# Kernel optimization log

Measured on AMD Instinct MI355X. Metric: run time of the kernel, lower is better.

Reference implementation:

```python
import jax, jax.numpy as jnp
import numpy as np

N = 30000      # num_nodes
R0 = 8         # original relations
R = 2 * R0 + 1 # with inverses + self-loop relation = 17
IN = 256
OUT = 256
E = 300000     # original triples
NB = 8         # num_bases


def setup_inputs() -> dict:
    key = jax.random.key(0)
    k1, k2, k3, k4, k5, k6 = jax.random.split(key, 6)
    s = jax.random.randint(k1, (E,), 0, N)
    r = jax.random.randint(k2, (E,), 0, R0)
    o = jax.random.randint(k3, (E,), 0, N)
    triples = jnp.stack([s, r, o], axis=1)  # [E,3] int
    features = jax.random.normal(k4, (N, IN), dtype=jnp.float32)
    bases = jax.random.normal(k5, (NB, IN, OUT), dtype=jnp.float32) * 0.02
    comps = jax.random.normal(k6, (R, NB), dtype=jnp.float32) * 0.02
    bias = jnp.zeros((OUT,), dtype=jnp.float32)
    return {"triples": triples, "features": features, "bases": bases, "comps": comps, "bias": bias}


def reference(triples, features, bases, comps, bias):
    # basis decomposition: weights[r] = sum_b comps[r,b] * bases[b]
    weights = jnp.einsum('rb,bio->rio', comps, bases)  # [R, IN, OUT]

    s, r, o = triples[:, 0], triples[:, 1], triples[:, 2]
    nodes = jnp.arange(N)
    # eval mode: self_loop_keep_prob = 1 -> all N self loops kept
    src = jnp.concatenate([s, o, nodes])                                  # [E + E + N]
    rel = jnp.concatenate([r, r + R0, jnp.full((N,), 2 * R0, r.dtype)])
    dst = jnp.concatenate([o, s, nodes])

    # horizontal stacking: adj is [N, R*N]; row = src, col = rel*N + dst
    cols = rel * N + dst
    # column normalisation (row_normalisation=False branch of sum_sparse)
    col_sums = jnp.zeros((R * N,), jnp.float32).at[cols].add(1.0)
    sums = col_sums[cols]
    # reorder: swap normalizers of original and inverse edge blocks
    sums = jnp.concatenate([sums[E:2 * E], sums[:E], sums[2 * E:]])
    vals = 1.0 / sums

    # fw[r*N + n] = features[n] @ weights[r]
    fw = jnp.einsum('ni,rio->rno', features, weights).reshape(R * N, OUT)
    msgs = vals[:, None] * fw[cols]                    # [num_edges, OUT]
    out = jnp.zeros((N, OUT), jnp.float32).at[src].add(msgs)
    return out + bias
```

## Files before the change

### kernel.cpp

```cpp
#include <hip/hip_runtime.h>


namespace {
constexpr int kN     = 30000;
constexpr int kR0    = 8;
constexpr int kNRel  = 16;
constexpr int kIN    = 256;
constexpr int kOUT   = 256;
constexpr int kE     = 300000;
constexpr int kNB    = 8;
constexpr int kKT    = kNB * kIN;
constexpr int kRows  = kN * kNRel;
constexpr int kMsgs  = 2 * kE;
constexpr int kScanBlk  = 1024;
constexpr int kNScanBlk = (kRows + kScanBlk - 1) / kScanBlk;
constexpr int kBM    = 64;
constexpr int kMB    = (kN + kBM - 1) / kBM;
constexpr int kMPad  = kMB * kBM;
constexpr int kTN    = 16;
}

typedef __bf16 bf16x8 __attribute__((ext_vector_type(8)));
typedef float  f32x4  __attribute__((ext_vector_type(4)));
typedef float  f32x2  __attribute__((ext_vector_type(2)));
typedef float  f32x4v __attribute__((ext_vector_type(4)));
typedef unsigned int u32;

static __device__ __forceinline__ ushort f2bf(float x) {
  unsigned u = __float_as_uint(x);
  u += 0x7FFF + ((u >> 16) & 1);
  return (ushort)(u >> 16);
}

static __device__ __forceinline__ void gload16(const void* g, void* l) {
  __builtin_amdgcn_global_load_lds(
      (const __attribute__((address_space(1))) u32*)g,
      (__attribute__((address_space(3))) u32*)l, 16, 0, 0);
}

#define PKFMA_LO(ACC, G, C) \
  asm("v_pk_fma_f32 %0, %1, %2, %0 op_sel_hi:[1,0,1]" : "+v"(ACC) : "v"(G), "v"(C))
#define PKFMA_HI(ACC, G, C) \
  asm("v_pk_fma_f32 %0, %1, %2, %0 op_sel:[0,1,0] op_sel_hi:[1,1,1]" : "+v"(ACC) : "v"(G), "v"(C))


__global__ void k_prep(const float* __restrict__ f, ushort* __restrict__ fb,
                       const int* __restrict__ t, int* __restrict__ deg) {
  int i = blockIdx.x * 256 + threadIdx.x;
  if (i < kN * kIN / 4) {
    float4 v = reinterpret_cast<const float4*>(f)[i];
    ushort4 p;
    p.x = f2bf(v.x); p.y = f2bf(v.y); p.z = f2bf(v.z); p.w = f2bf(v.w);
    reinterpret_cast<ushort4*>(fb)[i] = p;
  }
  if (i < kE) {
    int s = t[3*i], r = t[3*i+1], o = t[3*i+2];
    atomicAdd(&deg[s * kNRel + r], 1);
    atomicAdd(&deg[o * kNRel + kR0 + r], 1);
  }
}

__global__ void k_bt(const float* __restrict__ bases, ushort* __restrict__ Bt) {
  __shared__ float tile[16][256];
  int b = blockIdx.x;
  int t = threadIdx.x;
#pragma unroll
  for (int kk = 0; kk < 16; ++kk)
    tile[kk][t] = bases[(size_t)(b * 16 + kk) * kOUT + t];
  __syncthreads();
  char* dst = (char*)Bt + (size_t)t * 4096;
  int xr = (t & 7) << 4;
#pragma unroll
  for (int q = 0; q < 4; ++q) {
    ushort4 p;
    p.x = f2bf(tile[q*4+0][t]); p.y = f2bf(tile[q*4+1][t]);
    p.z = f2bf(tile[q*4+2][t]); p.w = f2bf(tile[q*4+3][t]);
    *reinterpret_cast<ushort4*>(dst + ((b * 32 + q * 8) ^ xr)) = p;
  }
}


__global__ void k_scan1(const int* __restrict__ deg, int* __restrict__ rp,
                        int* __restrict__ blksum) {
  __shared__ int s[256];
  int tid = threadIdx.x;
  int base = blockIdx.x * kScanBlk + tid * 4;
  int v0 = 0, v1 = 0, v2 = 0, v3 = 0;
  if (base + 3 < kRows) {
    v0 = deg[base]; v1 = deg[base+1]; v2 = deg[base+2]; v3 = deg[base+3];
  } else {
    if (base     < kRows) v0 = deg[base];
    if (base + 1 < kRows) v1 = deg[base+1];
    if (base + 2 < kRows) v2 = deg[base+2];
  }
  int t0 = v0, t1 = t0 + v1, t2 = t1 + v2, t3 = t2 + v3;
  s[tid] = t3;
  __syncthreads();
  for (int off = 1; off < 256; off <<= 1) {
    int x = 0;
    if (tid >= off) x = s[tid - off];
    __syncthreads();
    s[tid] += x;
    __syncthreads();
  }
  int excl = tid ? s[tid-1] : 0;
  if (base     < kRows) rp[base]   = excl;
  if (base + 1 < kRows) rp[base+1] = excl + t0;
  if (base + 2 < kRows) rp[base+2] = excl + t1;
  if (base + 3 < kRows) rp[base+3] = excl + t2;
  if (tid == 255) blksum[blockIdx.x] = s[255];
}

__global__ void k_scan2(int* __restrict__ blksum) {
  __shared__ int s[512];
  int tid = threadIdx.x;
  s[tid] = (tid < kNScanBlk) ? blksum[tid] : 0;
  __syncthreads();
  for (int off = 1; off < 512; off <<= 1) {
    int x = 0;
    if (tid >= off) x = s[tid - off];
    __syncthreads();
    s[tid] += x;
    __syncthreads();
  }
  if (tid < kNScanBlk) blksum[tid] = tid ? s[tid-1] : 0;
}

__global__ void k_scan3(int* __restrict__ rp, const int* __restrict__ blksum) {
  int i = blockIdx.x * 256 + threadIdx.x;
  if (i < kRows)       rp[i] += blksum[i >> 10];
  else if (i == kRows) rp[i]  = kMsgs;
}

__global__ void k_scatter(const int* __restrict__ t, const int* __restrict__ rp,
                          int* __restrict__ deg, int* __restrict__ col) {
  int m = blockIdx.x * 256 + threadIdx.x;
  if (m >= kMsgs) return;
  int e = (m < kE) ? m : m - kE;
  int s = t[3*e], r = t[3*e+1], o = t[3*e+2];
  int rr, tn, sn;
  if (m < kE) { rr = r;        tn = s; sn = o; }
  else        { rr = kR0 + r;  tn = o; sn = s; }
  int idx = tn * kNRel + rr;
  int pos = rp[idx] + (atomicSub(&deg[idx], 1) - 1);
  col[pos] = (rr << 16) | sn;
}

#define FMA4(A, S, G) \
  A.x += (S) * G.x; A.y += (S) * G.y; A.z += (S) * G.z; A.w += (S) * G.w;


__global__ __launch_bounds__(256, 6)
void k_agg1(const int* __restrict__ rp, const int* __restrict__ col,
            const ushort* __restrict__ featbf, const float* __restrict__ comps,
            ushort* __restrict__ aggb) {
  __shared__ float cvb[4][17][kNB];
  int wv   = threadIdx.x >> 6;
  int lane = threadIdx.x & 63;
  int node = blockIdx.x * 4 + wv;

  if (lane < 17) {
    float val = 0.f;
    if (lane < kNRel) {
      int idx = node * kNRel + lane;
      int d = rp[idx + 1] - rp[idx];
      val = d > 0 ? 1.0f / (float)d : 0.f;
    }
#pragma unroll
    for (int b = 0; b < kNB; ++b)
      cvb[wv][lane][b] = comps[lane * kNB + b] * val;
  }
  __syncthreads();

  int se0 = __builtin_amdgcn_readfirstlane(rp[node * kNRel]);
  int se1 = __builtin_amdgcn_readfirstlane(rp[node * kNRel + kNRel]);

  f32x2 accp[2 * kNB];
  {
    uint2 sf = *reinterpret_cast<const uint2*>(featbf + (size_t)node * kIN + lane * 4);
    f32x2 p01, p23;
    p01.x = __uint_as_float(sf.x << 16);
    p01.y = __uint_as_float(sf.x & 0xFFFF0000u);
    p23.x = __uint_as_float(sf.y << 16);
    p23.y = __uint_as_float(sf.y & 0xFFFF0000u);
#pragma unroll
    for (int b = 0; b < kNB; ++b) {
      float cs = comps[2*kR0*kNB + b];
      accp[2*b]     = p01 * cs;
      accp[2*b + 1] = p23 * cs;
    }
  }

  const int pad = (16 << 16);
  int voff = lane * 4;

  int sc[4];
#pragma unroll
  for (int j = 0; j < 4; ++j) {
    int ee = se0 + j;
    int ic = ee < se1 ? ee : 0;
    int v  = col[ic];
    sc[j] = ee < se1 ? v : pad;
  }

  for (int e = se0; e < se1; e += 4) {
    uint2 g[4];
#pragma unroll
    for (int j = 0; j < 4; ++j) {
      const ushort* rowp = featbf + (size_t)(sc[j] & 0xFFFF) * kIN;
      g[j] = *reinterpret_cast<const uint2*>(rowp + voff);
    }
    int sr[4];
#pragma unroll
    for (int j = 0; j < 4; ++j) sr[j] = sc[j] >> 16;
#pragma unroll
    for (int j = 0; j < 4; ++j) {
      int ee = e + 4 + j;
      int ic = ee < se1 ? ee : 0;
      int v  = col[ic];
      sc[j] = ee < se1 ? v : pad;
    }
#pragma unroll
    for (int j = 0; j < 4; ++j) {
      f32x4v cA = *reinterpret_cast<const f32x4v*>(&cvb[wv][sr[j]][0]);
      f32x4v cB = *reinterpret_cast<const f32x4v*>(&cvb[wv][sr[j]][4]);
      f32x2 p01, p23;
      p01.x = __uint_as_float(g[j].x << 16);
      p01.y = __uint_as_float(g[j].x & 0xFFFF0000u);
      p23.x = __uint_as_float(g[j].y << 16);
      p23.y = __uint_as_float(g[j].y & 0xFFFF0000u);
      f32x2 cAl = cA.lo, cAh = cA.hi, cBl = cB.lo, cBh = cB.hi;
      PKFMA_LO(accp[0],  p01, cAl); PKFMA_LO(accp[1],  p23, cAl);
      PKFMA_HI(accp[2],  p01, cAl); PKFMA_HI(accp[3],  p23, cAl);
      PKFMA_LO(accp[4],  p01, cAh); PKFMA_LO(accp[5],  p23, cAh);
      PKFMA_HI(accp[6],  p01, cAh); PKFMA_HI(accp[7],  p23, cAh);
      PKFMA_LO(accp[8],  p01, cBl); PKFMA_LO(accp[9],  p23, cBl);
      PKFMA_HI(accp[10], p01, cBl); PKFMA_HI(accp[11], p23, cBl);
      PKFMA_LO(accp[12], p01, cBh); PKFMA_LO(accp[13], p23, cBh);
      PKFMA_HI(accp[14], p01, cBh); PKFMA_HI(accp[15], p23, cBh);
    }
  }

  char* rowp = (char*)aggb + (size_t)node * 4096;
  int xr = (node & 7) << 4;
#pragma unroll
  for (int b = 0; b < kNB; ++b) {
    ushort4 p;
    p.x = f2bf(accp[2*b].x);     p.y = f2bf(accp[2*b].y);
    p.z = f2bf(accp[2*b + 1].x); p.w = f2bf(accp[2*b + 1].y);
    *reinterpret_cast<ushort4*>(rowp + ((b * 512 + lane * 8) ^ xr)) = p;
  }
}


__global__ __launch_bounds__(512, 4)
void k_gemm(const ushort* __restrict__ aggb, const ushort* __restrict__ Bt,
            const float* __restrict__ bias, float* __restrict__ out) {
  __shared__ ushort Albs[2][kBM * 64];
  __shared__ ushort Blds[2][256 * 64];
  int tid  = threadIdx.x;
  int wv   = tid >> 6;
  int lane = tid & 63;
  int mh   = wv >> 2;
  int nq   = wv & 3;
  int l15  = lane & 15;
  int g4   = lane >> 4;
  int node0 = blockIdx.x * kBM;

  f32x4 acc[2][4];
#pragma unroll
  for (int mt = 0; mt < 2; ++mt)
#pragma unroll
    for (int nt = 0; nt < 4; ++nt) acc[mt][nt] = f32x4{0.f, 0.f, 0.f, 0.f};

  auto stage = [&](int c, int buf) {
    {
      int lin = wv * 1024 + lane * 16;
      int row = lin >> 7;
      const char* src = (const char*)aggb + (size_t)(node0 + row) * 4096
                        + c * 128 + (lin & 127);
      gload16(src, (char*)Albs[buf] + wv * 1024);
    }
#pragma unroll
    for (int i = 0; i < 4; ++i) {
      int seg = wv * 4 + i;
      int lin = seg * 1024 + lane * 16;
      int colr = lin >> 7;
      const char* src = (const char*)Bt + (size_t)colr * 4096
                        + c * 128 + (lin & 127);
      gload16(src, (char*)Blds[buf] + seg * 1024);
    }
  };

  stage(0, 0);
  asm volatile("s_waitcnt vmcnt(0)" ::: "memory");
  __syncthreads();

  int cur = 0;
  for (int c = 0; c < 32; ++c) {
    if (c + 1 < 32) stage(c + 1, cur ^ 1);
#pragma unroll
    for (int ks = 0; ks < 2; ++ks) {
      int kb = ks * 64 + g4 * 16;
      bf16x8 a[2], b[4];
#pragma unroll
      for (int mt = 0; mt < 2; ++mt) {
        int row = mh * 32 + mt * 16 + l15;
        a[mt] = *reinterpret_cast<const bf16x8*>(
            (const char*)Albs[cur] + row * 128 + (kb ^ ((row & 7) << 4)));
      }
#pragma unroll
      for (int nt = 0; nt < 4; ++nt) {
        int colr = nq * 64 + nt * 16 + l15;
        b[nt] = *reinterpret_cast<const bf16x8*>(
            (const char*)Blds[cur] + colr * 128 + (kb ^ ((colr & 7) << 4)));
      }
#pragma unroll
      for (int mt = 0; mt < 2; ++mt)
#pragma unroll
        for (int nt = 0; nt < 4; ++nt)
          acc[mt][nt] = __builtin_amdgcn_mfma_f32_16x16x32_bf16(a[mt], b[nt],
                                                                acc[mt][nt], 0, 0, 0);
    }
    asm volatile("s_waitcnt vmcnt(0)" ::: "memory");
    __syncthreads();
    cur ^= 1;
  }

#pragma unroll
  for (int nt = 0; nt < 4; ++nt) {
    int colo = nq * 64 + nt * 16 + l15;
    float bi = bias[colo];
#pragma unroll
    for (int mt = 0; mt < 2; ++mt) {
      int rbase = node0 + mh * 32 + mt * 16 + g4 * 4;
#pragma unroll
      for (int j = 0; j < 4; ++j) {
        int row = rbase + j;
        if (row < kN) out[(size_t)row * kOUT + colo] = acc[mt][nt][j] + bi;
      }
    }
  }
}


__global__ __launch_bounds__(512, 4)
void k_out_fused(const int* __restrict__ rp, const int* __restrict__ col,
                 const float* __restrict__ feat, const ushort* __restrict__ featbf,
                 const ushort* __restrict__ Bt, const float* __restrict__ comps,
                 const float* __restrict__ bias, float* __restrict__ out) {
  __shared__ ushort aggs[kTN * kKT];
  __shared__ float  cvb[kTN][17][kNB];
  int tid  = threadIdx.x;
  int wv   = tid >> 6;
  int lane = tid & 63;
  int node0 = blockIdx.x * kTN;

  for (int q = tid; q < kTN * 17; q += 512) {
    int nl = q / 17, rl = q - nl * 17;
    float val = 0.f;
    if (rl < kNRel) {
      int idx = (node0 + nl) * kNRel + rl;
      int d = rp[idx + 1] - rp[idx];
      val = d > 0 ? 1.0f / (float)d : 0.f;
    }
#pragma unroll
    for (int b = 0; b < kNB; ++b)
      cvb[nl][rl][b] = comps[rl * kNB + b] * val;
  }
  __syncthreads();

  for (int half = 0; half < 2; ++half) {
    int nl   = (wv << 1) | half;
    int node = node0 + nl;
    int e0 = rp[node * kNRel];
    int e1 = rp[node * kNRel + kNRel];

    float4 f = *reinterpret_cast<const float4*>(feat + (size_t)node * kIN + lane * 4);
    float4 acc[kNB];
#pragma unroll
    for (int b = 0; b < kNB; ++b) {
      float cs = comps[2*kR0*kNB + b];
      acc[b].x = cs * f.x; acc[b].y = cs * f.y; acc[b].z = cs * f.z; acc[b].w = cs * f.w;
    }
    const float4* cvr = reinterpret_cast<const float4*>(&cvb[nl][0][0]);
    const int pad = (16 << 16);
    int cc[4];
#pragma unroll
    for (int j = 0; j < 4; ++j) {
      int ee = e0 + j;
      int v  = col[ee < kMsgs ? ee : kMsgs - 1];
      cc[j] = ee < e1 ? v : pad;
    }
    for (int e = e0; e < e1; e += 4) {
      uint2 g[4];
#pragma unroll
      for (int j = 0; j < 4; ++j) {
        int sn = cc[j] & 0xFFFF;
        g[j] = *reinterpret_cast<const uint2*>(featbf + (size_t)sn * kIN + lane * 4);
      }
      int rr[4];
#pragma unroll
      for (int j = 0; j < 4; ++j) rr[j] = cc[j] >> 16;
#pragma unroll
      for (int j = 0; j < 4; ++j) {
        int ee = e + 4 + j;
        int v  = col[ee < kMsgs ? ee : kMsgs - 1];
        cc[j] = ee < e1 ? v : pad;
      }
#pragma unroll
      for (int j = 0; j < 4; ++j) {
        float4 c0 = cvr[rr[j] * 2];
        float4 c1 = cvr[rr[j] * 2 + 1];
        float4 gg;
        gg.x = __uint_as_float(g[j].x << 16);
        gg.y = __uint_as_float(g[j].x & 0xFFFF0000u);
        gg.z = __uint_as_float(g[j].y << 16);
        gg.w = __uint_as_float(g[j].y & 0xFFFF0000u);
        FMA4(acc[0], c0.x, gg) FMA4(acc[1], c0.y, gg)
        FMA4(acc[2], c0.z, gg) FMA4(acc[3], c0.w, gg)
        FMA4(acc[4], c1.x, gg) FMA4(acc[5], c1.y, gg)
        FMA4(acc[6], c1.z, gg) FMA4(acc[7], c1.w, gg)
      }
    }
    int xr = (nl & 7) << 4;
#pragma unroll
    for (int b = 0; b < kNB; ++b) {
      ushort4 p;
      p.x = f2bf(acc[b].x); p.y = f2bf(acc[b].y);
      p.z = f2bf(acc[b].z); p.w = f2bf(acc[b].w);
      int byteoff = nl * 4096 + ((b * 512 + lane * 8) ^ xr);
      *reinterpret_cast<ushort4*>(reinterpret_cast<char*>(aggs) + byteoff) = p;
    }
  }
  __syncthreads();

  {
    int n  = lane & 15;
    int g4 = lane >> 4;
    const char* abase = reinterpret_cast<const char*>(aggs) + n * 4096;
    int axor = (n & 7) << 4;
#pragma unroll
    for (int t = 0; t < 2; ++t) {
      int ntile = wv + t * 8;
      float bi = bias[ntile * 16 + n];
      const char* btrow = reinterpret_cast<const char*>(Bt)
                          + (size_t)(ntile * 16 + n) * 4096;
      int bxor = (n & 7) << 4;
      f32x4 acc = {0.f, 0.f, 0.f, 0.f};
#pragma unroll 4
      for (int ks = 0; ks < kKT / 32; ++ks) {
        int kb = ks * 64 + g4 * 16;
        bf16x8 af = *reinterpret_cast<const bf16x8*>(abase + (kb ^ axor));
        bf16x8 bf = *reinterpret_cast<const bf16x8*>(btrow + (kb ^ bxor));
        acc = __builtin_amdgcn_mfma_f32_16x16x32_bf16(af, bf, acc, 0, 0, 0);
      }
#pragma unroll
      for (int j = 0; j < 4; ++j) {
        int row = g4 * 4 + j;
        out[(size_t)(node0 + row) * kOUT + ntile * 16 + n] = acc[j] + bi;
      }
    }
  }
}


extern "C" void kernel_launch(void* const* d_in, const int* in_sizes, int n_in,
                              void* d_out, int out_size, void* d_ws, size_t ws_size,
                              hipStream_t stream) {
  const int*   triples = (const int*)  d_in[0];
  const float* feat    = (const float*)d_in[1];
  const float* bases   = (const float*)d_in[2];
  const float* comps   = (const float*)d_in[3];
  const float* bias    = (const float*)d_in[4];
  float* out = (float*)d_out;

  size_t featbf_b = (size_t)kN * kIN * 2;
  size_t bt_b     = (size_t)kOUT * kKT * 2;
  size_t aggb_b   = (size_t)kMPad * kKT * 2;
  size_t csr_b    = (size_t)(kRows + kRows + 1 + kMsgs + kNScanBlk) * 4;
  bool bigws = ws_size >= featbf_b + bt_b + aggb_b + csr_b + 1024;

  char* p = (char*)d_ws;
  ushort* featbf = (ushort*)p;            p += featbf_b;
  ushort* Bt     = (ushort*)p;            p += bt_b;
  ushort* aggb   = nullptr;
  if (bigws) { aggb = (ushort*)p;         p += aggb_b; }
  int* deg    = (int*)p;
  int* rp     = deg + kRows;
  int* col    = rp + kRows + 1;
  int* blksum = col + kMsgs;

  hipMemsetAsync(deg, 0, kRows * sizeof(int), stream);
  k_prep  <<<(kN * kIN / 4 + 255) / 256, 256, 0, stream>>>(feat, featbf, triples, deg);
  k_bt    <<<kKT / 16,            256, 0, stream>>>(bases, Bt);
  k_scan1 <<<kNScanBlk,           256, 0, stream>>>(deg, rp, blksum);
  k_scan2 <<<1,                   512, 0, stream>>>(blksum);
  k_scan3 <<<(kRows + 256) / 256, 256, 0, stream>>>(rp, blksum);
  k_scatter<<<(kMsgs + 255) / 256, 256, 0, stream>>>(triples, rp, deg, col);

  if (bigws) {
    k_agg1<<<kN / 4,  256, 0, stream>>>(rp, col, featbf, comps, aggb);
    k_gemm<<<kMB,     512, 0, stream>>>(aggb, Bt, bias, out);
  } else {
    k_out_fused<<<kN / kTN, 512, 0, stream>>>(rp, col, feat, featbf, Bt,
                                              comps, bias, out);
  }
}
```

Before: 182.7 us.

## Fuse bases conversion into prep, drop scan2, double-buffer agg gathers

Folds the bases-to-bf16 transpose into the prep kernel and removes the single-block second scan pass. Each scan3 block now reduces the preceding block sums itself, which cuts two kernel launches at the cost of redundant reduction work. The aggregation loop is restructured to software-pipeline feature gathers one batch of four edges ahead. The bf16 output stores become nontemporal. Together these aim to cut launch overhead and hide gather latency, at the cost of more registers and uncoalesced bases reads.

Measured after the change: 195.5 us. 1.07x slower.

```diff
diff --git a/kernel.cpp b/kernel.cpp
--- a/kernel.cpp
+++ b/kernel.cpp
@@ -45,7 +45,8 @@
 
 
 __global__ void k_prep(const float* __restrict__ f, ushort* __restrict__ fb,
-                       const int* __restrict__ t, int* __restrict__ deg) {
+                       const int* __restrict__ t, int* __restrict__ deg,
+                       const float* __restrict__ bases, ushort* __restrict__ Bt) {
   int i = blockIdx.x * 256 + threadIdx.x;
   if (i < kN * kIN / 4) {
     float4 v = reinterpret_cast<const float4*>(f)[i];
@@ -58,24 +59,21 @@
     atomicAdd(&deg[s * kNRel + r], 1);
     atomicAdd(&deg[o * kNRel + kR0 + r], 1);
   }
-}
-
-__global__ void k_bt(const float* __restrict__ bases, ushort* __restrict__ Bt) {
-  __shared__ float tile[16][256];
-  int b = blockIdx.x;
-  int t = threadIdx.x;
-#pragma unroll
-  for (int kk = 0; kk < 16; ++kk)
-    tile[kk][t] = bases[(size_t)(b * 16 + kk) * kOUT + t];
-  __syncthreads();
-  char* dst = (char*)Bt + (size_t)t * 4096;
-  int xr = (t & 7) << 4;
-#pragma unroll
-  for (int q = 0; q < 4; ++q) {
-    ushort4 p;
-    p.x = f2bf(tile[q*4+0][t]); p.y = f2bf(tile[q*4+1][t]);
-    p.z = f2bf(tile[q*4+2][t]); p.w = f2bf(tile[q*4+3][t]);
-    *reinterpret_cast<ushort4*>(dst + ((b * 32 + q * 8) ^ xr)) = p;
+  if (blockIdx.x < kKT / 16) {
+    int b  = blockIdx.x;
+    int tt = threadIdx.x;
+    char* dst = (char*)Bt + (size_t)tt * 4096;
+    int xr = (tt & 7) << 4;
+#pragma unroll
+    for (int q = 0; q < 4; ++q) {
+      int k0 = b * 16 + q * 4;
+      ushort4 p;
+      p.x = f2bf(bases[(size_t)(k0 + 0) * kOUT + tt]);
+      p.y = f2bf(bases[(size_t)(k0 + 1) * kOUT + tt]);
+      p.z = f2bf(bases[(size_t)(k0 + 2) * kOUT + tt]);
+      p.w = f2bf(bases[(size_t)(k0 + 3) * kOUT + tt]);
+      *reinterpret_cast<ushort4*>(dst + ((b * 32 + q * 8) ^ xr)) = p;
+    }
   }
 }
 
@@ -111,24 +109,23 @@
   if (tid == 255) blksum[blockIdx.x] = s[255];
 }
 
-__global__ void k_scan2(int* __restrict__ blksum) {
-  __shared__ int s[512];
+__global__ void k_scan3(int* __restrict__ rp, const int* __restrict__ blksum) {
+  __shared__ int red[256];
   int tid = threadIdx.x;
-  s[tid] = (tid < kNScanBlk) ? blksum[tid] : 0;
+  int B   = blockIdx.x;
+  int region = (B * 256) >> 10;
+  int partial = 0;
+  for (int k = tid; k < region; k += 256) partial += blksum[k];
+  red[tid] = partial;
   __syncthreads();
-  for (int off = 1; off < 512; off <<= 1) {
-    int x = 0;
-    if (tid >= off) x = s[tid - off];
+#pragma unroll
+  for (int off = 128; off > 0; off >>= 1) {
+    if (tid < off) red[tid] += red[tid + off];
     __syncthreads();
-    s[tid] += x;
-    __syncthreads();
-  }
-  if (tid < kNScanBlk) blksum[tid] = tid ? s[tid-1] : 0;
-}
-
-__global__ void k_scan3(int* __restrict__ rp, const int* __restrict__ blksum) {
-  int i = blockIdx.x * 256 + threadIdx.x;
-  if (i < kRows)       rp[i] += blksum[i >> 10];
+  }
+  int base = red[0];
+  int i = B * 256 + tid;
+  if (i < kRows)       rp[i] += base;
   else if (i == kRows) rp[i]  = kMsgs;
 }
 
@@ -193,37 +190,14 @@
 
   const int pad = (16 << 16);
   int voff = lane * 4;
-
-  int sc[4];
-#pragma unroll
-  for (int j = 0; j < 4; ++j) {
-    int ee = se0 + j;
-    int ic = ee < se1 ? ee : 0;
-    int v  = col[ic];
-    sc[j] = ee < se1 ? v : pad;
-  }
-
-  for (int e = se0; e < se1; e += 4) {
-    uint2 g[4];
+  const f32x4v* cvr = reinterpret_cast<const f32x4v*>(&cvb[wv][0][0]);
+
+  auto compute = [&](const uint2* g, const int* sc) {
 #pragma unroll
     for (int j = 0; j < 4; ++j) {
-      const ushort* rowp = featbf + (size_t)(sc[j] & 0xFFFF) * kIN;
-      g[j] = *reinterpret_cast<const uint2*>(rowp + voff);
-    }
-    int sr[4];
-#pragma unroll
-    for (int j = 0; j < 4; ++j) sr[j] = sc[j] >> 16;
-#pragma unroll
-    for (int j = 0; j < 4; ++j) {
-      int ee = e + 4 + j;
-      int ic = ee < se1 ? ee : 0;
-      int v  = col[ic];
-      sc[j] = ee < se1 ? v : pad;
-    }
-#pragma unroll
-    for (int j = 0; j < 4; ++j) {
-      f32x4v cA = *reinterpret_cast<const f32x4v*>(&cvb[wv][sr[j]][0]);
-      f32x4v cB = *reinterpret_cast<const f32x4v*>(&cvb[wv][sr[j]][4]);
+      int sr = sc[j] >> 16;
+      f32x4v cA = cvr[sr * 2];
+      f32x4v cB = cvr[sr * 2 + 1];
       f32x2 p01, p23;
       p01.x = __uint_as_float(g[j].x << 16);
       p01.y = __uint_as_float(g[j].x & 0xFFFF0000u);
@@ -239,16 +213,56 @@
       PKFMA_LO(accp[12], p01, cBh); PKFMA_LO(accp[13], p23, cBh);
       PKFMA_HI(accp[14], p01, cBh); PKFMA_HI(accp[15], p23, cBh);
     }
-  }
+  };
+
+  int sc0[4], sc1[4];
+  uint2 g0[4];
+#pragma unroll
+  for (int j = 0; j < 4; ++j) {
+    int ee = se0 + j;
+    int ic = ee < se1 ? ee : 0;
+    int v  = col[ic];
+    sc0[j] = ee < se1 ? v : pad;
+  }
+#pragma unroll
+  for (int j = 0; j < 4; ++j)
+    g0[j] = *reinterpret_cast<const uint2*>(featbf + (size_t)(sc0[j] & 0xFFFF) * kIN + voff);
+#pragma unroll
+  for (int j = 0; j < 4; ++j) {
+    int ee = se0 + 4 + j;
+    int ic = ee < se1 ? ee : 0;
+    int v  = col[ic];
+    sc1[j] = ee < se1 ? v : pad;
+  }
+
+  for (int e = se0; e + 4 < se1; e += 4) {
+    uint2 g1[4];
+#pragma unroll
+    for (int j = 0; j < 4; ++j)
+      g1[j] = *reinterpret_cast<const uint2*>(featbf + (size_t)(sc1[j] & 0xFFFF) * kIN + voff);
+    int sc2[4];
+#pragma unroll
+    for (int j = 0; j < 4; ++j) {
+      int ee = e + 8 + j;
+      int ic = ee < se1 ? ee : 0;
+      int v  = col[ic];
+      sc2[j] = ee < se1 ? v : pad;
+    }
+    compute(g0, sc0);
+#pragma unroll
+    for (int j = 0; j < 4; ++j) { g0[j] = g1[j]; sc0[j] = sc1[j]; sc1[j] = sc2[j]; }
+  }
+  if (se0 < se1) compute(g0, sc0);
 
   char* rowp = (char*)aggb + (size_t)node * 4096;
   int xr = (node & 7) << 4;
 #pragma unroll
   for (int b = 0; b < kNB; ++b) {
-    ushort4 p;
-    p.x = f2bf(accp[2*b].x);     p.y = f2bf(accp[2*b].y);
-    p.z = f2bf(accp[2*b + 1].x); p.w = f2bf(accp[2*b + 1].y);
-    *reinterpret_cast<ushort4*>(rowp + ((b * 512 + lane * 8) ^ xr)) = p;
+    union { ushort4 s; unsigned long long u; } cv;
+    cv.s.x = f2bf(accp[2*b].x);     cv.s.y = f2bf(accp[2*b].y);
+    cv.s.z = f2bf(accp[2*b + 1].x); cv.s.w = f2bf(accp[2*b + 1].y);
+    __builtin_nontemporal_store(cv.u,
+        reinterpret_cast<unsigned long long*>(rowp + ((b * 512 + lane * 8) ^ xr)));
   }
 }
 
@@ -492,12 +506,11 @@
   int* blksum = col + kMsgs;
 
   hipMemsetAsync(deg, 0, kRows * sizeof(int), stream);
-  k_prep  <<<(kN * kIN / 4 + 255) / 256, 256, 0, stream>>>(feat, featbf, triples, deg);
-  k_bt    <<<kKT / 16,            256, 0, stream>>>(bases, Bt);
-  k_scan1 <<<kNScanBlk,           256, 0, stream>>>(deg, rp, blksum);
-  k_scan2 <<<1,                   512, 0, stream>>>(blksum);
-  k_scan3 <<<(kRows + 256) / 256, 256, 0, stream>>>(rp, blksum);
-  k_scatter<<<(kMsgs + 255) / 256, 256, 0, stream>>>(triples, rp, deg, col);
+  k_prep  <<<(kN * kIN / 4 + 255) / 256, 256, 0, stream>>>(feat, featbf, triples, deg,
+                                                           bases, Bt);
+  k_scan1 <<<kNScanBlk,             256, 0, stream>>>(deg, rp, blksum);
+  k_scan3 <<<(kRows + 256) / 256,   256, 0, stream>>>(rp, blksum);
+  k_scatter<<<(kMsgs + 255) / 256,  256, 0, stream>>>(triples, rp, deg, col);
 
   if (bigws) {
     k_agg1<<<kN / 4,  256, 0, stream>>>(rp, col, featbf, comps, aggb);
```
